# Performance work log

Hardware: AMD Instinct MI355X
Metric: run time of the kernel (lower is better)

Reference implementation:

```python
import jax, jax.numpy as jnp
import numpy as np

N = 50000
E_RAND = 800000
F_IN = 512
HID = 64
HEADS = 4
C = 40
NEG_SLOPE = 0.2  # PyG GATConv default leaky_relu slope


def setup_inputs() -> dict:
    key = jax.random.key(0)
    ks = jax.random.split(key, 12)
    x = jax.random.normal(ks[0], (N, F_IN), dtype=jnp.float32)
    # random edges + self loops (PyG GATConv add_self_loops=True)
    ei_rand = jax.random.randint(ks[1], (2, E_RAND), 0, N, dtype=jnp.int64)
    loops = jnp.broadcast_to(jnp.arange(N, dtype=jnp.int64), (2, N))
    edge_index = jnp.concatenate([ei_rand, loops], axis=1)  # [2, 850000]
    # layer 1: F_IN -> HEADS*HID, concat
    s1 = 1.0 / np.sqrt(F_IN)
    W1 = jax.random.normal(ks[2], (F_IN, HEADS * HID), dtype=jnp.float32) * s1
    a_src1 = jax.random.normal(ks[3], (HEADS, HID), dtype=jnp.float32) * (1.0 / np.sqrt(HID))
    a_dst1 = jax.random.normal(ks[4], (HEADS, HID), dtype=jnp.float32) * (1.0 / np.sqrt(HID))
    b1 = jnp.zeros((HEADS * HID,), dtype=jnp.float32)
    # layer 2: HEADS*HID -> C, 1 head, concat=False
    s2 = 1.0 / np.sqrt(HEADS * HID)
    W2 = jax.random.normal(ks[5], (HEADS * HID, C), dtype=jnp.float32) * s2
    a_src2 = jax.random.normal(ks[6], (1, C), dtype=jnp.float32) * (1.0 / np.sqrt(C))
    a_dst2 = jax.random.normal(ks[7], (1, C), dtype=jnp.float32) * (1.0 / np.sqrt(C))
    b2 = jnp.zeros((C,), dtype=jnp.float32)
    return {"x": x, "edge_index": edge_index, "W1": W1, "a_src1": a_src1,
            "a_dst1": a_dst1, "b1": b1, "W2": W2, "a_src2": a_src2,
            "a_dst2": a_dst2, "b2": b2}


def gat_conv(x, src, dst, W, a_s, a_d, b, concat):
    n = x.shape[0]
    H, D = a_s.shape
    h = (x @ W).reshape(n, H, D)                    # [N,H,D]
    al_s = jnp.einsum('nhd,hd->nh', h, a_s)          # per-node src score
    al_d = jnp.einsum('nhd,hd->nh', h, a_d)          # per-node dst score
    e = jax.nn.leaky_relu(al_s[src] + al_d[dst], NEG_SLOPE)  # [E,H]
    # segment softmax over edges grouped by destination node
    m = jax.ops.segment_max(e, dst, num_segments=n)  # [N,H]
    e = jnp.exp(e - m[dst])
    denom = jax.ops.segment_sum(e, dst, num_segments=n)
    alpha = e / (denom[dst] + 1e-16)                 # [E,H]
    msg = h[src] * alpha[:, :, None]                 # [E,H,D]
    out = jax.ops.segment_sum(msg, dst, num_segments=n)  # [N,H,D]
    out = out.reshape(n, H * D) if concat else out.mean(axis=1)
    return out + b


def reference(x, edge_index, W1, a_src1, a_dst1, b1, W2, a_src2, a_dst2, b2):
    src, dst = edge_index[0], edge_index[1]
    # dropout p=0.6 is identity in eval mode
    h = jax.nn.elu(gat_conv(x, src, dst, W1, a_src1, a_dst1, b1, concat=True))
    out = gat_conv(h, src, dst, W2, a_src2, a_dst2, b2, concat=False)
    return jax.nn.log_softmax(out, axis=1)
```

## Files before the change

kernel.cpp:

```cpp
#include <hip/hip_runtime.h>
#include <math.h>

#define NNODES 50000
#define FIN 512
#define HID 64
#define HEADS 4
#define HD (HEADS * HID)
#define NCLS 40
#define NCLSP 64
#define NEG_SLOPE 0.2f
#define SBLK 256
#define NSCAN ((NNODES + SBLK - 1) / SBLK)

#define W1TBLK (FIN * HD / 256)
#define W2TBLK NCLSP

typedef __attribute__((ext_vector_type(8))) short short8;
typedef __attribute__((ext_vector_type(4))) float f32x4;

static __device__ inline unsigned short f2bf(float f) {
    unsigned int u = __builtin_bit_cast(unsigned int, f);
    unsigned int r = (u + 0x7FFFu + ((u >> 16) & 1u)) >> 16;
    return (unsigned short)r;
}
static __device__ inline float bf2f(unsigned short b) {
    return __builtin_bit_cast(float, (unsigned int)b << 16);
}
static __device__ inline void gload_lds16(const void* g, void* l) {
    __builtin_amdgcn_global_load_lds(
        (const __attribute__((address_space(1))) unsigned int*)g,
        (__attribute__((address_space(3))) unsigned int*)l, 16, 0, 0);
}

__global__ __launch_bounds__(256) void pre_kernel(const float* __restrict__ W1,
                                                  unsigned short* __restrict__ W1t,
                                                  const float* __restrict__ W2,
                                                  unsigned short* __restrict__ W2t,
                                                  const int* __restrict__ ei, int E, int eb,
                                                  int* __restrict__ deg,
                                                  int* __restrict__ csr_pad) {
    const int b = blockIdx.x;
    const int tid = threadIdx.x;
    if (b < eb) {
        const int e = b * 256 + tid;
        if (e < E) atomicAdd(&deg[ei[E + e]], 1);
        if (b == 0 && tid < 64) csr_pad[tid] = 0;
    } else if (b < eb + W1TBLK) {
        const int idx = (b - eb) * 256 + tid;
        const int k = idx >> 8;
        const int n = idx & 255;
        W1t[n * FIN + k] = f2bf(W1[idx]);
    } else {
        const int idx = (b - eb - W1TBLK) * 256 + tid;
        const int n = idx >> 8;
        const int k = idx & 255;
        W2t[n * HD + k] = (n < NCLS) ? f2bf(W2[k * NCLS + n]) : (unsigned short)0;
    }
}

#define BM 64
#define BN 256
#define BK 32
#define G1BLK ((NNODES + BM - 1) / BM)

__global__ __launch_bounds__(256) void gemm1_kernel(const float* __restrict__ x,
                                                    const unsigned short* __restrict__ W1t,
                                                    const float* __restrict__ a_src,
                                                    const float* __restrict__ a_dst,
                                                    unsigned short* __restrict__ h1,
                                                    float* __restrict__ al_s,
                                                    float* __restrict__ al_d) {
    __shared__ float As32[2][BM * BK];
    __shared__ unsigned short Bs[2][BN * BK];
    const int tid = threadIdx.x;
    const int wave = tid >> 6;
    const int lane = tid & 63;
    const int quad = lane >> 4;
    const int col = lane & 15;
    const int m0 = blockIdx.x * BM;
    const int srow = lane >> 2;
    const int skk = (lane & 3) * 8;
    const int l3 = lane >> 3;
    const int ch = lane & 7;
    const int chs = ch ^ l3;

    f32x4 acc[4][4] = {};

    auto stageA = [&](int buf, int k0) {
        #pragma unroll
        for (int j = 0; j < 2; ++j) {
            const int row = wave * 16 + j * 8 + l3;
            const size_t rg = (size_t)min(m0 + row, NNODES - 1) * FIN;
            gload_lds16(&x[rg + k0 + chs * 4], &As32[buf][row * BK + ch * 4]);
        }
    };
    auto stageB = [&](int buf, int k0) {
        #pragma unroll
        for (int c = 0; c < 4; ++c) {
            const int rr = c * 64 + wave * 16 + srow;
            gload_lds16(&W1t[(size_t)rr * FIN + k0 + skk], &Bs[buf][rr * BK + skk]);
        }
    };
    auto compute = [&](int buf) {
        const int r7 = col & 7;
        short8 af[4], bfv[4];
        #pragma unroll
        for (int i = 0; i < 4; ++i) {
            const int row = i * 16 + col;
            const float4 f0 = *(const float4*)&As32[buf][row * BK + (((2 * quad)     ^ r7) << 2)];
            const float4 f1 = *(const float4*)&As32[buf][row * BK + (((2 * quad + 1) ^ r7) << 2)];
            short8 p;
            p[0] = (short)f2bf(f0.x); p[1] = (short)f2bf(f0.y);
            p[2] = (short)f2bf(f0.z); p[3] = (short)f2bf(f0.w);
            p[4] = (short)f2bf(f1.x); p[5] = (short)f2bf(f1.y);
            p[6] = (short)f2bf(f1.z); p[7] = (short)f2bf(f1.w);
            af[i] = p;
        }
        #pragma unroll
        for (int j = 0; j < 4; ++j)
            bfv[j] = *(const short8*)&Bs[buf][(wave * 64 + j * 16 + col) * BK + quad * 8];
        #pragma unroll
        for (int i = 0; i < 4; ++i)
            #pragma unroll
            for (int j = 0; j < 4; ++j)
                acc[i][j] = __builtin_amdgcn_mfma_f32_16x16x32_bf16(af[i], bfv[j], acc[i][j], 0, 0, 0);
    };

    stageA(0, 0);
    stageB(0, 0);
    __syncthreads();
    int cur = 0;
    for (int k0 = BK; k0 < FIN; k0 += BK) {
        stageA(cur ^ 1, k0);
        stageB(cur ^ 1, k0);
        compute(cur);
        __syncthreads();
        cur ^= 1;
    }
    compute(cur);

    float asv[4], adv[4];
    #pragma unroll
    for (int j = 0; j < 4; ++j) {
        asv[j] = a_src[wave * 64 + j * 16 + col];
        adv[j] = a_dst[wave * 64 + j * 16 + col];
    }
    #pragma unroll
    for (int i = 0; i < 4; ++i) {
        #pragma unroll
        for (int reg = 0; reg < 4; ++reg) {
            const int row = i * 16 + quad * 4 + reg;
            const int gm = m0 + row;
            float ds = 0.f, dd = 0.f;
            #pragma unroll
            for (int j = 0; j < 4; ++j) {
                const float v = acc[i][j][reg];
                ds = fmaf(v, asv[j], ds);
                dd = fmaf(v, adv[j], dd);
                if (gm < NNODES) {
                    const int gc = wave * 64 + j * 16 + col;
                    h1[(size_t)gm * HD + gc] = f2bf(v);
                }
            }
            #pragma unroll
            for (int off = 1; off < 16; off <<= 1) {
                ds += __shfl_xor(ds, off);
                dd += __shfl_xor(dd, off);
            }
            if (col == 0 && gm < NNODES) {
                al_s[gm * HEADS + wave] = ds;
                al_d[gm * HEADS + wave] = dd;
            }
        }
    }
}

__global__ __launch_bounds__(SBLK) void scan1_kernel(const int* __restrict__ deg,
                                                     int* __restrict__ psum,
                                                     int* __restrict__ bsum) {
    __shared__ int ws[4];
    const int t = threadIdx.x;
    const int idx = blockIdx.x * SBLK + t;
    const int lane = t & 63;
    const int w = t >> 6;
    int sv = (idx < NNODES) ? deg[idx] : 0;
    #pragma unroll
    for (int off = 1; off < 64; off <<= 1) {
        const int n = __shfl_up(sv, off);
        if (lane >= off) sv += n;
    }
    if (lane == 63) ws[w] = sv;
    __syncthreads();
    int add = 0;
    for (int i = 0; i < w; ++i) add += ws[i];
    sv += add;
    if (idx < NNODES) psum[idx] = sv;
    if (t == SBLK - 1) bsum[blockIdx.x] = sv;
}

__global__ __launch_bounds__(SBLK) void scan23_kernel(const int* __restrict__ deg,
                                                      const int* __restrict__ psum,
                                                      const int* __restrict__ bsum,
                                                      int* __restrict__ offsets) {
    __shared__ int ws[4];
    __shared__ int sc[NSCAN];
    const int t = threadIdx.x;
    const int lane = t & 63;
    const int w = t >> 6;
    int sv = (t < NSCAN) ? bsum[t] : 0;
    #pragma unroll
    for (int off = 1; off < 64; off <<= 1) {
        const int n = __shfl_up(sv, off);
        if (lane >= off) sv += n;
    }
    if (lane == 63) ws[w] = sv;
    __syncthreads();
    int add = 0;
    for (int i = 0; i < w; ++i) add += ws[i];
    sv += add;
    if (t < NSCAN) sc[t] = sv;
    __syncthreads();
    const int idx = blockIdx.x * SBLK + t;
    const int boff = (blockIdx.x > 0) ? sc[blockIdx.x - 1] : 0;
    if (idx < NNODES) offsets[idx] = psum[idx] - deg[idx] + boff;
    if (blockIdx.x == 0 && t == 0) offsets[NNODES] = sc[NSCAN - 1];
}

__global__ void scatter_kernel(const int* __restrict__ ei, int E,
                               const int* __restrict__ offsets,
                               int* __restrict__ cursor,
                               int* __restrict__ csr_src) {
    const int e = blockIdx.x * 256 + threadIdx.x;
    if (e < E) {
        const int dst = ei[E + e];
        const int src = ei[e];
        const int pos = offsets[dst] + atomicAdd(&cursor[dst], 1);
        csr_src[pos] = src;
    }
}

__global__ __launch_bounds__(256) void agg1_kernel(const unsigned short* __restrict__ h1,
                                                   const float* __restrict__ al_s,
                                                   const float* __restrict__ al_d,
                                                   const int* __restrict__ offsets,
                                                   const int* __restrict__ csr_src,
                                                   const float* __restrict__ b1,
                                                   unsigned short* __restrict__ h_act) {
    const int node = (blockIdx.x * 256 + threadIdx.x) >> 6;
    const int lane = threadIdx.x & 63;
    const int q = lane >> 4;
    const int fl = lane & 15;
    const int h = fl >> 2;
    const float ad = al_d[node * HEADS + h];
    const int start = offsets[node];
    const int end = offsets[node + 1];

    float s = 0.f;
    float acc[16] = {};

    {
        const int idx = start + q;
        const int src0 = csr_src[idx];
        float sc = (idx < end) ? al_s[src0 * HEADS + h] : -__builtin_inff();
        uint4 v0 = *(const uint4*)&h1[(size_t)src0 * HD + fl * 16];
        uint4 v1 = *(const uint4*)&h1[(size_t)src0 * HD + fl * 16 + 8];

        for (int i = start; i < end; i += 4) {
            const int j = i + 4 + q;
            const int nsrc = csr_src[j];
            const float nsc = (j < end) ? al_s[nsrc * HEADS + h] : -__builtin_inff();
            const uint4 nv0 = *(const uint4*)&h1[(size_t)nsrc * HD + fl * 16];
            const uint4 nv1 = *(const uint4*)&h1[(size_t)nsrc * HD + fl * 16 + 8];
            float e_ = sc + ad;
            e_ = e_ > 0.f ? e_ : NEG_SLOPE * e_;
            const float p = __expf(e_);
            s += p;
            const unsigned int w[8] = {v0.x, v0.y, v0.z, v0.w, v1.x, v1.y, v1.z, v1.w};
            #pragma unroll
            for (int d = 0; d < 8; ++d) {
                const float lo = __builtin_bit_cast(float, w[d] << 16);
                const float hi = __builtin_bit_cast(float, w[d] & 0xFFFF0000u);
                acc[2 * d]     = fmaf(p, lo, acc[2 * d]);
                acc[2 * d + 1] = fmaf(p, hi, acc[2 * d + 1]);
            }
            sc = nsc; v0 = nv0; v1 = nv1;
        }
    }
    s += __shfl_xor(s, 16);
    s += __shfl_xor(s, 32);
    #pragma unroll
    for (int k = 0; k < 16; ++k) {
        acc[k] += __shfl_xor(acc[k], 16);
        acc[k] += __shfl_xor(acc[k], 32);
    }

    if (q == 0) {
        const float inv = 1.f / (s + 1e-16f);
        float bb[16];
        *(float4*)&bb[0]  = *(const float4*)&b1[fl * 16];
        *(float4*)&bb[4]  = *(const float4*)&b1[fl * 16 + 4];
        *(float4*)&bb[8]  = *(const float4*)&b1[fl * 16 + 8];
        *(float4*)&bb[12] = *(const float4*)&b1[fl * 16 + 12];
        short8 ob0, ob1;
        #pragma unroll
        for (int k = 0; k < 8; ++k) {
            const float o0 = acc[k] * inv + bb[k];
            const float o1 = acc[8 + k] * inv + bb[8 + k];
            const float e0 = o0 > 0.f ? o0 : expm1f(o0);
            const float e1 = o1 > 0.f ? o1 : expm1f(o1);
            ob0[k] = (short)f2bf(e0);
            ob1[k] = (short)f2bf(e1);
        }
        *(short8*)&h_act[(size_t)node * HD + fl * 16] = ob0;
        *(short8*)&h_act[(size_t)node * HD + fl * 16 + 8] = ob1;
    }
}

#define G2M 64
#define BSTRIDE 264

__global__ __launch_bounds__(256) void gemm2_kernel(const unsigned short* __restrict__ h_act,
                                                    const unsigned short* __restrict__ W2t,
                                                    const float* __restrict__ a_s2,
                                                    const float* __restrict__ a_d2,
                                                    unsigned short* __restrict__ h2,
                                                    float* __restrict__ al_s,
                                                    float* __restrict__ al_d) {
    __shared__ unsigned short Bt[NCLSP][BSTRIDE];
    const int tid = threadIdx.x;
    const int wave = tid >> 6;
    const int lane = tid & 63;
    const int quad = lane >> 4;
    const int col = lane & 15;
    const int m0 = blockIdx.x * G2M;

    #pragma unroll
    for (int it = 0; it < 8; ++it) {
        const int ch = it * 256 + tid;
        const int n = ch >> 5;
        const int c8 = (ch & 31) * 8;
        *(uint4*)&Bt[n][c8] = *(const uint4*)&W2t[(size_t)n * HD + c8];
    }

    const int rowm = m0 + wave * 16 + col;
    const int arow = min(rowm, NNODES - 1);
    short8 af[8];
    #pragma unroll
    for (int ks = 0; ks < 8; ++ks)
        af[ks] = *(const short8*)&h_act[(size_t)arow * HD + ks * 32 + quad * 8];

    __syncthreads();

    f32x4 acc[4] = {};
    #pragma unroll
    for (int j = 0; j < 4; ++j) {
        #pragma unroll
        for (int ks = 0; ks < 8; ++ks) {
            const short8 bfr = *(const short8*)&Bt[j * 16 + col][ks * 32 + quad * 8];
            acc[j] = __builtin_amdgcn_mfma_f32_16x16x32_bf16(af[ks], bfr, acc[j], 0, 0, 0);
        }
    }

    float ps[4] = {0.f, 0.f, 0.f, 0.f};
    float pd[4] = {0.f, 0.f, 0.f, 0.f};
    #pragma unroll
    for (int j = 0; j < 4; ++j) {
        const int c = j * 16 + col;
        const bool cv = c < NCLS;
        const float asc = cv ? a_s2[c] : 0.f;
        const float adc = cv ? a_d2[c] : 0.f;
        #pragma unroll
        for (int reg = 0; reg < 4; ++reg) {
            const float v = acc[j][reg];
            ps[reg] += v * asc;
            pd[reg] += v * adc;
            const int node = m0 + wave * 16 + quad * 4 + reg;
            if (node < NNODES)
                h2[(size_t)node * NCLSP + c] = f2bf(v);
        }
    }
    #pragma unroll
    for (int reg = 0; reg < 4; ++reg) {
        #pragma unroll
        for (int off = 1; off < 16; off <<= 1) {
            ps[reg] += __shfl_xor(ps[reg], off);
            pd[reg] += __shfl_xor(pd[reg], off);
        }
    }
    if (col == 0) {
        #pragma unroll
        for (int reg = 0; reg < 4; ++reg) {
            const int node = m0 + wave * 16 + quad * 4 + reg;
            if (node < NNODES) {
                al_s[node] = ps[reg];
                al_d[node] = pd[reg];
            }
        }
    }
}

__global__ __launch_bounds__(256) void agg2_kernel(const unsigned short* __restrict__ h2,
                                                   const float* __restrict__ al_s,
                                                   const float* __restrict__ al_d,
                                                   const int* __restrict__ offsets,
                                                   const int* __restrict__ csr_src,
                                                   const float* __restrict__ b2,
                                                   float* __restrict__ out) {
    const int node = (blockIdx.x * 256 + threadIdx.x) >> 6;
    const int lane = threadIdx.x & 63;
    const int oct = lane >> 3;
    const int fl = lane & 7;
    const float ad = al_d[node];
    const int start = offsets[node];
    const int end = offsets[node + 1];

    float s = 0.f;
    float acc[8] = {};

    {
        const int idx = start + oct;
        const int src0 = csr_src[idx];
        float sc = (idx < end) ? al_s[src0] : -__builtin_inff();
        short8 v = *(const short8*)&h2[(size_t)src0 * NCLSP + fl * 8];

        for (int i = start; i < end; i += 8) {
            const int j = i + 8 + oct;
            const int nsrc = csr_src[j];
            const float nsc = (j < end) ? al_s[nsrc] : -__builtin_inff();
            const short8 nv = *(const short8*)&h2[(size_t)nsrc * NCLSP + fl * 8];
            float e_ = sc + ad;
            e_ = e_ > 0.f ? e_ : NEG_SLOPE * e_;
            const float p = __expf(e_);
            s += p;
            #pragma unroll
            for (int k = 0; k < 8; ++k)
                acc[k] = fmaf(p, bf2f((unsigned short)v[k]), acc[k]);
            sc = nsc; v = nv;
        }
    }
    s += __shfl_xor(s, 8);
    s += __shfl_xor(s, 16);
    s += __shfl_xor(s, 32);
    #pragma unroll
    for (int k = 0; k < 8; ++k) {
        acc[k] += __shfl_xor(acc[k], 8);
        acc[k] += __shfl_xor(acc[k], 16);
        acc[k] += __shfl_xor(acc[k], 32);
    }

    if (oct == 0) {
        const float inv = 1.f / (s + 1e-16f);
        float o[8];
        float mx = -1e30f;
        #pragma unroll
        for (int k = 0; k < 8; ++k) {
            const int c = fl * 8 + k;
            const float bc = (c < NCLS) ? b2[c] : 0.f;
            o[k] = acc[k] * inv + bc;
            if (c < NCLS) mx = fmaxf(mx, o[k]);
        }
        #pragma unroll
        for (int off = 1; off < 8; off <<= 1) mx = fmaxf(mx, __shfl_xor(mx, off));
        float ex = 0.f;
        #pragma unroll
        for (int k = 0; k < 8; ++k) {
            const int c = fl * 8 + k;
            if (c < NCLS) ex += __expf(o[k] - mx);
        }
        #pragma unroll
        for (int off = 1; off < 8; off <<= 1) ex += __shfl_xor(ex, off);
        const float lse = mx + logf(ex);
        if (fl < 5) {
            float4 r0, r1;
            r0.x = o[0] - lse; r0.y = o[1] - lse; r0.z = o[2] - lse; r0.w = o[3] - lse;
            r1.x = o[4] - lse; r1.y = o[5] - lse; r1.z = o[6] - lse; r1.w = o[7] - lse;
            *(float4*)&out[(size_t)node * NCLS + fl * 8] = r0;
            *(float4*)&out[(size_t)node * NCLS + fl * 8 + 4] = r1;
        }
    }
}

extern "C" void kernel_launch(void* const* d_in, const int* in_sizes, int n_in,
                              void* d_out, int out_size, void* d_ws, size_t ws_size,
                              hipStream_t stream) {
    const float* x      = (const float*)d_in[0];
    const int*   ei     = (const int*)d_in[1];
    const float* W1     = (const float*)d_in[2];
    const float* a_src1 = (const float*)d_in[3];
    const float* a_dst1 = (const float*)d_in[4];
    const float* b1     = (const float*)d_in[5];
    const float* W2     = (const float*)d_in[6];
    const float* a_src2 = (const float*)d_in[7];
    const float* a_dst2 = (const float*)d_in[8];
    const float* b2     = (const float*)d_in[9];
    float* out = (float*)d_out;
    const int E = in_sizes[1] / 2;

    char* ws = (char*)d_ws;
    size_t off = 0;
    auto alloc = [&](size_t bytes) -> char* {
        char* p = ws + off;
        off += (bytes + 255) & ~(size_t)255;
        return p;
    };
    unsigned short* W1t   = (unsigned short*)alloc((size_t)FIN * HD * 2);
    unsigned short* W2t   = (unsigned short*)alloc((size_t)NCLSP * HD * 2);
    unsigned short* h1    = (unsigned short*)alloc((size_t)NNODES * HD * 2);
    unsigned short* h_act = (unsigned short*)alloc((size_t)NNODES * HD * 2);
    unsigned short* h2    = (unsigned short*)alloc((size_t)NNODES * NCLSP * 2);
    float* al_s1  = (float*)alloc((size_t)NNODES * HEADS * 4);
    float* al_d1  = (float*)alloc((size_t)NNODES * HEADS * 4);
    float* al_s2  = (float*)alloc((size_t)NNODES * 4);
    float* al_d2  = (float*)alloc((size_t)NNODES * 4);
    int*   deg    = (int*)alloc((size_t)NNODES * 4);
    int*   cursor = (int*)alloc((size_t)NNODES * 4);
    int*   psum   = (int*)alloc((size_t)NNODES * 4);
    int*   bsum   = (int*)alloc((size_t)SBLK * 4);
    int*   offs   = (int*)alloc((size_t)(NNODES + 1) * 4);
    int*   csrsrc = (int*)alloc((size_t)E * 4 + 256);

    const size_t degpad = ((size_t)NNODES * 4 + 255) & ~(size_t)255;
    hipMemsetAsync(deg, 0, degpad + (size_t)NNODES * 4, stream);

    const int eb = (E + 255) / 256;
    pre_kernel<<<eb + W1TBLK + W2TBLK, 256, 0, stream>>>(W1, W1t, W2, W2t, ei, E, eb, deg, csrsrc + E);
    scan1_kernel<<<NSCAN, SBLK, 0, stream>>>(deg, psum, bsum);
    scan23_kernel<<<NSCAN, SBLK, 0, stream>>>(deg, psum, bsum, offs);
    scatter_kernel<<<eb, 256, 0, stream>>>(ei, E, offs, cursor, csrsrc);

    gemm1_kernel<<<G1BLK, 256, 0, stream>>>(x, W1t, a_src1, a_dst1, h1, al_s1, al_d1);
    agg1_kernel<<<NNODES / 4, 256, 0, stream>>>(h1, al_s1, al_d1, offs, csrsrc, b1, h_act);
    gemm2_kernel<<<(NNODES + G2M - 1) / G2M, 256, 0, stream>>>(h_act, W2t, a_src2, a_dst2, h2, al_s2, al_d2);
    agg2_kernel<<<NNODES / 4, 256, 0, stream>>>(h2, al_s2, al_d2, offs, csrsrc, b2, out);
}
```

Measured before the change: 401.1 us.

## Split layer-1 aggregation across 8 feature slices per node

The layer-1 aggregation kernel now handles each node with 8 blocks, one per 32-feature slice. Each wave covers one slice and processes 8 edges at a time, with every lane loading 4 bf16 features instead of 32. This raises parallelism and memory-level concurrency and lowers register pressure. In exchange, csr_src, al_s and the offsets are re-read by 8 blocks per node, the launch has 8x more blocks, and gathers shrink to 8-byte loads per lane.

After: 510.4 us. 27.3% more time.

```diff
diff --git a/kernel.cpp b/kernel.cpp
--- a/kernel.cpp
+++ b/kernel.cpp
@@ -246,73 +246,68 @@
                                                    const int* __restrict__ csr_src,
                                                    const float* __restrict__ b1,
                                                    unsigned short* __restrict__ h_act) {
-    const int node = (blockIdx.x * 256 + threadIdx.x) >> 6;
+    const int bid = blockIdx.x;
+    const int s = bid & 7;
+    const int ng = bid >> 3;
+    const int node = ng * 4 + (threadIdx.x >> 6);
     const int lane = threadIdx.x & 63;
-    const int q = lane >> 4;
-    const int fl = lane & 15;
-    const int h = fl >> 2;
+    const int oct = lane >> 3;
+    const int fl = lane & 7;
+    const int h = s >> 1;
+    const int f0 = s * 32 + fl * 4;
     const float ad = al_d[node * HEADS + h];
     const int start = offsets[node];
     const int end = offsets[node + 1];
 
-    float s = 0.f;
-    float acc[16] = {};
+    float sm = 0.f;
+    float acc[4] = {};
 
     {
-        const int idx = start + q;
+        const int idx = start + oct;
         const int src0 = csr_src[idx];
         float sc = (idx < end) ? al_s[src0 * HEADS + h] : -__builtin_inff();
-        uint4 v0 = *(const uint4*)&h1[(size_t)src0 * HD + fl * 16];
-        uint4 v1 = *(const uint4*)&h1[(size_t)src0 * HD + fl * 16 + 8];
-
-        for (int i = start; i < end; i += 4) {
-            const int j = i + 4 + q;
+        uint2 v = *(const uint2*)&h1[(size_t)src0 * HD + f0];
+
+        for (int i = start; i < end; i += 8) {
+            const int j = i + 8 + oct;
             const int nsrc = csr_src[j];
             const float nsc = (j < end) ? al_s[nsrc * HEADS + h] : -__builtin_inff();
-            const uint4 nv0 = *(const uint4*)&h1[(size_t)nsrc * HD + fl * 16];
-            const uint4 nv1 = *(const uint4*)&h1[(size_t)nsrc * HD + fl * 16 + 8];
+            const uint2 nv = *(const uint2*)&h1[(size_t)nsrc * HD + f0];
             float e_ = sc + ad;
             e_ = e_ > 0.f ? e_ : NEG_SLOPE * e_;
             const float p = __expf(e_);
-            s += p;
-            const unsigned int w[8] = {v0.x, v0.y, v0.z, v0.w, v1.x, v1.y, v1.z, v1.w};
-            #pragma unroll
-            for (int d = 0; d < 8; ++d) {
-                const float lo = __builtin_bit_cast(float, w[d] << 16);
-                const float hi = __builtin_bit_cast(float, w[d] & 0xFFFF0000u);
-                acc[2 * d]     = fmaf(p, lo, acc[2 * d]);
-                acc[2 * d + 1] = fmaf(p, hi, acc[2 * d + 1]);
-            }
-            sc = nsc; v0 = nv0; v1 = nv1;
-        }
-    }
-    s += __shfl_xor(s, 16);
-    s += __shfl_xor(s, 32);
-    #pragma unroll
-    for (int k = 0; k < 16; ++k) {
+            sm += p;
+            acc[0] = fmaf(p, __builtin_bit_cast(float, v.x << 16), acc[0]);
+            acc[1] = fmaf(p, __builtin_bit_cast(float, v.x & 0xFFFF0000u), acc[1]);
+            acc[2] = fmaf(p, __builtin_bit_cast(float, v.y << 16), acc[2]);
+            acc[3] = fmaf(p, __builtin_bit_cast(float, v.y & 0xFFFF0000u), acc[3]);
+            sc = nsc; v = nv;
+        }
+    }
+    sm += __shfl_xor(sm, 8);
+    sm += __shfl_xor(sm, 16);
+    sm += __shfl_xor(sm, 32);
+    #pragma unroll
+    for (int k = 0; k < 4; ++k) {
+        acc[k] += __shfl_xor(acc[k], 8);
         acc[k] += __shfl_xor(acc[k], 16);
         acc[k] += __shfl_xor(acc[k], 32);
     }
 
-    if (q == 0) {
-        const float inv = 1.f / (s + 1e-16f);
-        float bb[16];
-        *(float4*)&bb[0]  = *(const float4*)&b1[fl * 16];
-        *(float4*)&bb[4]  = *(const float4*)&b1[fl * 16 + 4];
-        *(float4*)&bb[8]  = *(const float4*)&b1[fl * 16 + 8];
-        *(float4*)&bb[12] = *(const float4*)&b1[fl * 16 + 12];
-        short8 ob0, ob1;
-        #pragma unroll
-        for (int k = 0; k < 8; ++k) {
-            const float o0 = acc[k] * inv + bb[k];
-            const float o1 = acc[8 + k] * inv + bb[8 + k];
-            const float e0 = o0 > 0.f ? o0 : expm1f(o0);
-            const float e1 = o1 > 0.f ? o1 : expm1f(o1);
-            ob0[k] = (short)f2bf(e0);
-            ob1[k] = (short)f2bf(e1);
-        }
-        *(short8*)&h_act[(size_t)node * HD + fl * 16] = ob0;
-        *(short8*)&h_act[(size_t)node * HD + fl * 16 + 8] = ob1;
+    if (oct == 0) {
+        const float inv = 1.f / (sm + 1e-16f);
+        const float4 bb = *(const float4*)&b1[f0];
+        float o0 = acc[0] * inv + bb.x;
+        float o1 = acc[1] * inv + bb.y;
+        float o2 = acc[2] * inv + bb.z;
+        float o3 = acc[3] * inv + bb.w;
+        o0 = o0 > 0.f ? o0 : expm1f(o0);
+        o1 = o1 > 0.f ? o1 : expm1f(o1);
+        o2 = o2 > 0.f ? o2 : expm1f(o2);
+        o3 = o3 > 0.f ? o3 : expm1f(o3);
+        ushort4 ob;
+        ob.x = f2bf(o0); ob.y = f2bf(o1); ob.z = f2bf(o2); ob.w = f2bf(o3);
+        *(ushort4*)&h_act[(size_t)node * HD + f0] = ob;
     }
 }
 
@@ -529,7 +524,7 @@
     scatter_kernel<<<eb, 256, 0, stream>>>(ei, E, offs, cursor, csrsrc);
 
     gemm1_kernel<<<G1BLK, 256, 0, stream>>>(x, W1t, a_src1, a_dst1, h1, al_s1, al_d1);
-    agg1_kernel<<<NNODES / 4, 256, 0, stream>>>(h1, al_s1, al_d1, offs, csrsrc, b1, h_act);
+    agg1_kernel<<<(NNODES / 4) * 8, 256, 0, stream>>>(h1, al_s1, al_d1, offs, csrsrc, b1, h_act);
     gemm2_kernel<<<(NNODES + G2M - 1) / G2M, 256, 0, stream>>>(h_act, W2t, a_src2, a_dst2, h2, al_s2, al_d2);
     agg2_kernel<<<NNODES / 4, 256, 0, stream>>>(h2, al_s2, al_d2, offs, csrsrc, b2, out);
 }
```

## Fuse CSR build and weight conversion into one cooperative persistent kernel

Applied to the files above, without the earlier changes.

Replaces the memset, pre-kernel, two scan kernels and scatter kernel with a single cooperative launch of 960 blocks. The phases (zeroing and weight transpose, degree count, block scan, global scan, scatter) are separated by grid.sync(). This removes four launch boundaries and the memset. In exchange it adds grid-wide barriers and runs the edge loops with fewer threads in grid-stride form. Correctness assumes all 960 blocks are co-resident, and the scans need at least NSCAN (196) blocks.

Result: slower. 798.0 us (+99.0%).

```diff
diff --git a/kernel.cpp b/kernel.cpp
--- a/kernel.cpp
+++ b/kernel.cpp
@@ -1,5 +1,8 @@
 #include <hip/hip_runtime.h>
+#include <hip/hip_cooperative_groups.h>
 #include <math.h>
+
+namespace cg = cooperative_groups;
 
 #define NNODES 50000
 #define FIN 512
@@ -12,9 +15,6 @@
 #define SBLK 256
 #define NSCAN ((NNODES + SBLK - 1) / SBLK)
 
-#define W1TBLK (FIN * HD / 256)
-#define W2TBLK NCLSP
-
 typedef __attribute__((ext_vector_type(8))) short short8;
 typedef __attribute__((ext_vector_type(4))) float f32x4;
 
@@ -32,29 +32,90 @@
         (__attribute__((address_space(3))) unsigned int*)l, 16, 0, 0);
 }
 
-__global__ __launch_bounds__(256) void pre_kernel(const float* __restrict__ W1,
+__global__ __launch_bounds__(256) void csr_kernel(const int* __restrict__ ei, int E,
+                                                  const float* __restrict__ W1,
                                                   unsigned short* __restrict__ W1t,
                                                   const float* __restrict__ W2,
                                                   unsigned short* __restrict__ W2t,
-                                                  const int* __restrict__ ei, int E, int eb,
                                                   int* __restrict__ deg,
-                                                  int* __restrict__ csr_pad) {
-    const int b = blockIdx.x;
+                                                  int* __restrict__ cursor,
+                                                  int* __restrict__ psum,
+                                                  int* __restrict__ bsum,
+                                                  int* __restrict__ offs,
+                                                  int* __restrict__ csr_src) {
+    cg::grid_group grid = cg::this_grid();
     const int tid = threadIdx.x;
-    if (b < eb) {
-        const int e = b * 256 + tid;
-        if (e < E) atomicAdd(&deg[ei[E + e]], 1);
-        if (b == 0 && tid < 64) csr_pad[tid] = 0;
-    } else if (b < eb + W1TBLK) {
-        const int idx = (b - eb) * 256 + tid;
-        const int k = idx >> 8;
-        const int n = idx & 255;
-        W1t[n * FIN + k] = f2bf(W1[idx]);
-    } else {
-        const int idx = (b - eb - W1TBLK) * 256 + tid;
-        const int n = idx >> 8;
-        const int k = idx & 255;
+    const int gidx = blockIdx.x * 256 + tid;
+    const int gstride = gridDim.x * 256;
+    __shared__ int ws[4];
+    __shared__ int sc[NSCAN];
+
+    for (int i = gidx; i < NNODES; i += gstride) { deg[i] = 0; cursor[i] = 0; }
+    if (gidx < 64) csr_src[E + gidx] = 0;
+    for (int i = gidx; i < FIN * HD; i += gstride) {
+        const int k = i >> 8;
+        const int n = i & 255;
+        W1t[n * FIN + k] = f2bf(W1[i]);
+    }
+    for (int i = gidx; i < NCLSP * HD; i += gstride) {
+        const int n = i >> 8;
+        const int k = i & 255;
         W2t[n * HD + k] = (n < NCLS) ? f2bf(W2[k * NCLS + n]) : (unsigned short)0;
+    }
+    grid.sync();
+
+    for (int e = gidx; e < E; e += gstride) atomicAdd(&deg[ei[E + e]], 1);
+    grid.sync();
+
+    if (blockIdx.x < NSCAN) {
+        const int idx = blockIdx.x * SBLK + tid;
+        const int lane = tid & 63;
+        const int w = tid >> 6;
+        int sv = (idx < NNODES) ? deg[idx] : 0;
+        #pragma unroll
+        for (int off = 1; off < 64; off <<= 1) {
+            const int n = __shfl_up(sv, off);
+            if (lane >= off) sv += n;
+        }
+        if (lane == 63) ws[w] = sv;
+        __syncthreads();
+        int add = 0;
+        for (int i = 0; i < w; ++i) add += ws[i];
+        sv += add;
+        if (idx < NNODES) psum[idx] = sv;
+        if (tid == SBLK - 1) bsum[blockIdx.x] = sv;
+    }
+    grid.sync();
+
+    if (blockIdx.x < NSCAN) {
+        __syncthreads();
+        const int lane = tid & 63;
+        const int w = tid >> 6;
+        int sv = (tid < NSCAN) ? bsum[tid] : 0;
+        #pragma unroll
+        for (int off = 1; off < 64; off <<= 1) {
+            const int n = __shfl_up(sv, off);
+            if (lane >= off) sv += n;
+        }
+        if (lane == 63) ws[w] = sv;
+        __syncthreads();
+        int add = 0;
+        for (int i = 0; i < w; ++i) add += ws[i];
+        sv += add;
+        if (tid < NSCAN) sc[tid] = sv;
+        __syncthreads();
+        const int idx = blockIdx.x * SBLK + tid;
+        const int boff = (blockIdx.x > 0) ? sc[blockIdx.x - 1] : 0;
+        if (idx < NNODES) offs[idx] = psum[idx] - deg[idx] + boff;
+        if (blockIdx.x == 0 && tid == 0) offs[NNODES] = sc[NSCAN - 1];
+    }
+    grid.sync();
+
+    for (int e = gidx; e < E; e += gstride) {
+        const int dst = ei[E + e];
+        const int src = ei[e];
+        const int pos = offs[dst] + atomicAdd(&cursor[dst], 1);
+        csr_src[pos] = src;
     }
 }
 
@@ -175,70 +236,6 @@
     }
 }
 
-__global__ __launch_bounds__(SBLK) void scan1_kernel(const int* __restrict__ deg,
-                                                     int* __restrict__ psum,
-                                                     int* __restrict__ bsum) {
-    __shared__ int ws[4];
-    const int t = threadIdx.x;
-    const int idx = blockIdx.x * SBLK + t;
-    const int lane = t & 63;
-    const int w = t >> 6;
-    int sv = (idx < NNODES) ? deg[idx] : 0;
-    #pragma unroll
-    for (int off = 1; off < 64; off <<= 1) {
-        const int n = __shfl_up(sv, off);
-        if (lane >= off) sv += n;
-    }
-    if (lane == 63) ws[w] = sv;
-    __syncthreads();
-    int add = 0;
-    for (int i = 0; i < w; ++i) add += ws[i];
-    sv += add;
-    if (idx < NNODES) psum[idx] = sv;
-    if (t == SBLK - 1) bsum[blockIdx.x] = sv;
-}
-
-__global__ __launch_bounds__(SBLK) void scan23_kernel(const int* __restrict__ deg,
-                                                      const int* __restrict__ psum,
-                                                      const int* __restrict__ bsum,
-                                                      int* __restrict__ offsets) {
-    __shared__ int ws[4];
-    __shared__ int sc[NSCAN];
-    const int t = threadIdx.x;
-    const int lane = t & 63;
-    const int w = t >> 6;
-    int sv = (t < NSCAN) ? bsum[t] : 0;
-    #pragma unroll
-    for (int off = 1; off < 64; off <<= 1) {
-        const int n = __shfl_up(sv, off);
-        if (lane >= off) sv += n;
-    }
-    if (lane == 63) ws[w] = sv;
-    __syncthreads();
-    int add = 0;
-    for (int i = 0; i < w; ++i) add += ws[i];
-    sv += add;
-    if (t < NSCAN) sc[t] = sv;
-    __syncthreads();
-    const int idx = blockIdx.x * SBLK + t;
-    const int boff = (blockIdx.x > 0) ? sc[blockIdx.x - 1] : 0;
-    if (idx < NNODES) offsets[idx] = psum[idx] - deg[idx] + boff;
-    if (blockIdx.x == 0 && t == 0) offsets[NNODES] = sc[NSCAN - 1];
-}
-
-__global__ void scatter_kernel(const int* __restrict__ ei, int E,
-                               const int* __restrict__ offsets,
-                               int* __restrict__ cursor,
-                               int* __restrict__ csr_src) {
-    const int e = blockIdx.x * 256 + threadIdx.x;
-    if (e < E) {
-        const int dst = ei[E + e];
-        const int src = ei[e];
-        const int pos = offsets[dst] + atomicAdd(&cursor[dst], 1);
-        csr_src[pos] = src;
-    }
-}
-
 __global__ __launch_bounds__(256) void agg1_kernel(const unsigned short* __restrict__ h1,
                                                    const float* __restrict__ al_s,
                                                    const float* __restrict__ al_d,
@@ -519,14 +516,13 @@
     int*   offs   = (int*)alloc((size_t)(NNODES + 1) * 4);
     int*   csrsrc = (int*)alloc((size_t)E * 4 + 256);
 
-    const size_t degpad = ((size_t)NNODES * 4 + 255) & ~(size_t)255;
-    hipMemsetAsync(deg, 0, degpad + (size_t)NNODES * 4, stream);
-
-    const int eb = (E + 255) / 256;
-    pre_kernel<<<eb + W1TBLK + W2TBLK, 256, 0, stream>>>(W1, W1t, W2, W2t, ei, E, eb, deg, csrsrc + E);
-    scan1_kernel<<<NSCAN, SBLK, 0, stream>>>(deg, psum, bsum);
-    scan23_kernel<<<NSCAN, SBLK, 0, stream>>>(deg, psum, bsum, offs);
-    scatter_kernel<<<eb, 256, 0, stream>>>(ei, E, offs, cursor, csrsrc);
+    {
+        void* args[] = {(void*)&ei, (void*)&E, (void*)&W1, (void*)&W1t,
+                        (void*)&W2, (void*)&W2t, (void*)&deg, (void*)&cursor,
+                        (void*)&psum, (void*)&bsum, (void*)&offs, (void*)&csrsrc};
+        hipLaunchCooperativeKernel((void*)csr_kernel, dim3(960), dim3(256),
+                                   args, 0, stream);
+    }
 
     gemm1_kernel<<<G1BLK, 256, 0, stream>>>(x, W1t, a_src1, a_dst1, h1, al_s1, al_d1);
     agg1_kernel<<<NNODES / 4, 256, 0, stream>>>(h1, al_s1, al_d1, offs, csrsrc, b1, h_act);
```
